# Kernel optimization log

Measured on AMD Instinct MI355X. Metric: run time of the kernel, lower is better.

The kernel has to match this reference:

```python
import jax, jax.numpy as jnp
from jax import lax
import numpy as np

N_E = 1024
E_DIM = 512
BETA = 0.25


def setup_inputs() -> dict:
    key = jax.random.key(0)
    k1, k2 = jax.random.split(key)
    z = jax.random.normal(k1, (16, 4096, E_DIM), dtype=jnp.float32)
    # torch init: uniform(-1/n_e, 1/n_e)
    codebook = jax.random.uniform(k2, (N_E, E_DIM), dtype=jnp.float32,
                                  minval=-1.0 / N_E, maxval=1.0 / N_E)
    return {"z": z, "codebook": codebook}


def reference(z, codebook):
    zf = z.reshape(-1, z.shape[-1])                      # (N, e_dim)
    # squared-distance matrix: ||z||^2 + ||e||^2 - 2 z e^T  -> (N, n_e)
    d = (jnp.sum(zf * zf, axis=1, keepdims=True)
         + jnp.sum(codebook * codebook, axis=1)
         - 2.0 * (zf @ codebook.T))
    idx = jnp.argmin(d, axis=1)                          # (N,)
    z_q = codebook[idx].reshape(z.shape)                 # (B, S, e_dim)
    loss = (jnp.mean((z_q - lax.stop_gradient(z)) ** 2)
            + BETA * jnp.mean((lax.stop_gradient(z_q) - z) ** 2))
    # straight-through estimator
    z_q_st = z + lax.stop_gradient(z_q - z)
    # perplexity of code usage (mean of one-hot == normalized counts)
    counts = jnp.zeros((codebook.shape[0],), dtype=z.dtype).at[idx].add(1.0)
    e_mean = counts / idx.shape[0]
    perplexity = jnp.exp(-jnp.sum(e_mean * jnp.log(e_mean + 1e-10)))
    return (loss, z_q_st, idx, perplexity)
```

## Files before the change

kernel.cpp:

```cpp
#include <hip/hip_runtime.h>
#include <hip/hip_bf16.h>

#define N_ROWS 65536
#define EDIM   512
#define NCODES 1024

#define WS_LOSS   0
#define WS_COUNTS 1
#define WS_ENORM  1025
#define WS_ZNORM  2049
#define WS_AMBCNT (2049 + 65536)
#define WS_WINNER (WS_AMBCNT + 1)
#define WS_AMBLST (WS_WINNER + 65536)
#define AMB_CAP   32768
#define WS_E2_OFF (1u << 20)
#define WS_FAST_BYTES (3u * 1024u * 1024u + 4096u)

#define AMB_EPS 1.6e-4f

typedef short short8 __attribute__((ext_vector_type(8)));
typedef float f32x4  __attribute__((ext_vector_type(4)));

#define AS1C(p) ((const __attribute__((address_space(1))) void*)(p))
#define AS3(p)  ((__attribute__((address_space(3))) void*)(p))

static __device__ __forceinline__ unsigned short f2bf(float f) {
    unsigned u = __float_as_uint(f);
    u += 0x7FFFu + ((u >> 16) & 1u);
    return (unsigned short)(u >> 16);
}
static __device__ __forceinline__ float bf2f(unsigned short h) {
    return __uint_as_float(((unsigned)h) << 16);
}

__global__ __launch_bounds__(256) void vq_prep(const float* __restrict__ cb,
                                               float* __restrict__ ws) {
    int j = blockIdx.x;
    int tid = threadIdx.x;
    float2 v = *(const float2*)&cb[(size_t)j * EDIM + tid * 2];
    float s = v.x * v.x + v.y * v.y;
    #pragma unroll
    for (int off = 32; off > 0; off >>= 1) s += __shfl_down(s, off);
    __shared__ float ls[4];
    int wave = tid >> 6, lane = tid & 63;
    if (lane == 0) ls[wave] = s;
    __syncthreads();
    if (tid == 0) {
        ws[WS_ENORM + j] = ls[0] + ls[1] + ls[2] + ls[3];
        ws[WS_COUNTS + j] = 0.0f;
        if (j == 0) {
            ws[WS_LOSS] = 0.0f;
            ((int*)ws)[WS_AMBCNT] = 0;
        }
    }
}

__global__ __launch_bounds__(256) void vq_znorm(const float* __restrict__ z,
                                                float* __restrict__ ws) {
    int tid  = threadIdx.x;
    int lrow = tid >> 5;
    int c    = tid & 31;
    long row = (long)blockIdx.x * 8 + lrow;
    const float* p = z + row * EDIM + (c >> 3) * 128 + (c & 7);
    float r = p[0] * p[0];
    #pragma unroll
    for (int i = 1; i < 16; ++i) {
        float v = p[i * 8];
        r += v * v;
    }
    r += __shfl_xor(r, 1);
    r += __shfl_xor(r, 2);
    r += __shfl_xor(r, 4);
    r += __shfl_xor(r, 8);
    r += __shfl_xor(r, 16);
    if (c == 0) ws[WS_ZNORM + row] = r;
}

__global__ __launch_bounds__(256) void vq_convz(const float* __restrict__ z,
                                                unsigned short* __restrict__ z2) {
    const int tid = threadIdx.x;
    const int p = blockIdx.x;
    const long row0 = (long)p * 128;
    const int row = tid >> 1, half = tid & 1;
    for (int kc = 0; kc < 16; ++kc) {
        const float* src = z + (row0 + row) * EDIM + kc * 32 + half * 16;
        float f[16];
        #pragma unroll
        for (int q = 0; q < 4; ++q) {
            float4 v = ((const float4*)src)[q];
            f[q*4+0] = v.x; f[q*4+1] = v.y; f[q*4+2] = v.z; f[q*4+3] = v.w;
        }
        unsigned hi[8], lo[8];
        #pragma unroll
        for (int q = 0; q < 8; ++q) {
            unsigned short h0 = f2bf(f[2*q]);
            unsigned short h1 = f2bf(f[2*q+1]);
            unsigned short l0 = f2bf(f[2*q]   - bf2f(h0));
            unsigned short l1 = f2bf(f[2*q+1] - bf2f(h1));
            hi[q] = (unsigned)h0 | ((unsigned)h1 << 16);
            lo[q] = (unsigned)l0 | ((unsigned)l1 << 16);
        }
        size_t base = ((size_t)(p * 16 + kc) * 2) * 4096;
        unsigned* dhi = (unsigned*)(z2 + base        + row * 32 + half * 16);
        unsigned* dlo = (unsigned*)(z2 + base + 4096 + row * 32 + half * 16);
        ((uint4*)dhi)[0] = make_uint4(hi[0], hi[1], hi[2], hi[3]);
        ((uint4*)dhi)[1] = make_uint4(hi[4], hi[5], hi[6], hi[7]);
        ((uint4*)dlo)[0] = make_uint4(lo[0], lo[1], lo[2], lo[3]);
        ((uint4*)dlo)[1] = make_uint4(lo[4], lo[5], lo[6], lo[7]);
    }
}

__global__ __launch_bounds__(256) void vq_convcb(const float* __restrict__ cb,
                                                 unsigned short* __restrict__ e2) {
    const int tid = threadIdx.x;
    const int cc = blockIdx.x;
    const int row = tid >> 1, half = tid & 1;
    for (int kc = 0; kc < 16; ++kc) {
        const float* src = cb + (size_t)(cc * 128 + row) * EDIM + kc * 32 + half * 16;
        float f[16];
        #pragma unroll
        for (int q = 0; q < 4; ++q) {
            float4 v = ((const float4*)src)[q];
            f[q*4+0] = v.x; f[q*4+1] = v.y; f[q*4+2] = v.z; f[q*4+3] = v.w;
        }
        unsigned hi[8], lo[8];
        #pragma unroll
        for (int q = 0; q < 8; ++q) {
            unsigned short h0 = f2bf(f[2*q]);
            unsigned short h1 = f2bf(f[2*q+1]);
            unsigned short l0 = f2bf(f[2*q]   - bf2f(h0));
            unsigned short l1 = f2bf(f[2*q+1] - bf2f(h1));
            hi[q] = (unsigned)h0 | ((unsigned)h1 << 16);
            lo[q] = (unsigned)l0 | ((unsigned)l1 << 16);
        }
        size_t base = ((size_t)(cc * 16 + kc) * 2) * 4096;
        unsigned* dhi = (unsigned*)(e2 + base        + row * 32 + half * 16);
        unsigned* dlo = (unsigned*)(e2 + base + 4096 + row * 32 + half * 16);
        ((uint4*)dhi)[0] = make_uint4(hi[0], hi[1], hi[2], hi[3]);
        ((uint4*)dhi)[1] = make_uint4(hi[4], hi[5], hi[6], hi[7]);
        ((uint4*)dlo)[0] = make_uint4(lo[0], lo[1], lo[2], lo[3]);
        ((uint4*)dlo)[1] = make_uint4(lo[4], lo[5], lo[6], lo[7]);
    }
}

__global__ __launch_bounds__(256, 2) void vq_mfma(const unsigned short* __restrict__ z2,
                                                  const unsigned short* __restrict__ e2,
                                                  const float* __restrict__ ws,
                                                  int* __restrict__ winner,
                                                  int* __restrict__ amb_count,
                                                  int* __restrict__ amb_list) {
    __shared__ unsigned short stage[16384];
    __shared__ float fv1[2][128];
    __shared__ float fv2[2][128];
    __shared__ int   fc1[2][128];

    const int tid = threadIdx.x;
    const int lane = tid & 63, w = tid >> 6;
    const int rw = (w & 1) * 64, cw = (w >> 1) * 64;
    const int ml = lane & 15, kg = lane >> 4;
    const long row0 = (long)blockIdx.x * 128;
    const float* __restrict__ enorm = ws + WS_ENORM;

    float v1[16], v2[16];
    int   c1[16];
    #pragma unroll
    for (int i = 0; i < 16; ++i) { v1[i] = INFINITY; v2[i] = INFINITY; c1[i] = 0; }

    const unsigned short* zt = stage;
    const unsigned short* et = stage + 8192;

    for (int cc = 0; cc < 8; ++cc) {
        f32x4 acc[4][4];
        #pragma unroll
        for (int rt = 0; rt < 4; ++rt)
            #pragma unroll
            for (int ct = 0; ct < 4; ++ct)
                acc[rt][ct] = (f32x4){0.f, 0.f, 0.f, 0.f};

        for (int kc = 0; kc < 16; ++kc) {
            __syncthreads();
            const uint4* zsrc = (const uint4*)(z2 + (size_t)(blockIdx.x * 16 + kc) * 8192);
            const uint4* esrc = (const uint4*)(e2 + (size_t)(cc * 16 + kc) * 8192);
            uint4* st = (uint4*)stage;
#if defined(__has_builtin) && __has_builtin(__builtin_amdgcn_global_load_lds)
            #pragma unroll
            for (int it = 0; it < 4; ++it) {
                int base = it * 256 + w * 64;
                __builtin_amdgcn_global_load_lds(AS1C(zsrc + base + lane), AS3(st + base), 16, 0, 0);
            }
            #pragma unroll
            for (int it = 0; it < 4; ++it) {
                int base = it * 256 + w * 64;
                __builtin_amdgcn_global_load_lds(AS1C(esrc + base + lane), AS3(st + 1024 + base), 16, 0, 0);
            }
#else
            #pragma unroll
            for (int it = 0; it < 4; ++it) {
                int i = it * 256 + tid;
                st[i] = zsrc[i];
            }
            #pragma unroll
            for (int it = 0; it < 4; ++it) {
                int i = it * 256 + tid;
                st[1024 + i] = esrc[i];
            }
#endif
            __syncthreads();

            short8 a[4][2], b[4][2];
            #pragma unroll
            for (int rt = 0; rt < 4; ++rt) {
                a[rt][0] = *(const short8*)&zt[        (rw + rt * 16 + ml) * 32 + kg * 8];
                a[rt][1] = *(const short8*)&zt[4096 + (rw + rt * 16 + ml) * 32 + kg * 8];
            }
            #pragma unroll
            for (int ct = 0; ct < 4; ++ct) {
                b[ct][0] = *(const short8*)&et[        (cw + ct * 16 + ml) * 32 + kg * 8];
                b[ct][1] = *(const short8*)&et[4096 + (cw + ct * 16 + ml) * 32 + kg * 8];
            }
            #pragma unroll
            for (int rt = 0; rt < 4; ++rt)
                #pragma unroll
                for (int ct = 0; ct < 4; ++ct) {
                    acc[rt][ct] = __builtin_amdgcn_mfma_f32_16x16x32_bf16(a[rt][0], b[ct][0], acc[rt][ct], 0, 0, 0);
                    acc[rt][ct] = __builtin_amdgcn_mfma_f32_16x16x32_bf16(a[rt][0], b[ct][1], acc[rt][ct], 0, 0, 0);
                    acc[rt][ct] = __builtin_amdgcn_mfma_f32_16x16x32_bf16(a[rt][1], b[ct][0], acc[rt][ct], 0, 0, 0);
                }
        }

        float en[4];
        #pragma unroll
        for (int ct = 0; ct < 4; ++ct) en[ct] = enorm[cc * 128 + cw + ct * 16 + ml];
        #pragma unroll
        for (int rt = 0; rt < 4; ++rt)
            #pragma unroll
            for (int ct = 0; ct < 4; ++ct) {
                int code = cc * 128 + cw + ct * 16 + ml;
                #pragma unroll
                for (int reg = 0; reg < 4; ++reg) {
                    float d = fmaf(-2.0f, acc[rt][ct][reg], en[ct]);
                    int i = rt * 4 + reg;
                    bool lt1 = d < v1[i];
                    bool lt2 = d < v2[i];
                    v2[i] = lt1 ? v1[i] : (lt2 ? d : v2[i]);
                    v1[i] = lt1 ? d : v1[i];
                    c1[i] = lt1 ? code : c1[i];
                }
            }
    }

    #pragma unroll
    for (int i = 0; i < 16; ++i) {
        #pragma unroll
        for (int off = 1; off < 16; off <<= 1) {
            float ov1 = __shfl_xor(v1[i], off);
            int   oc1 = __shfl_xor(c1[i], off);
            float ov2 = __shfl_xor(v2[i], off);
            bool take = (ov1 < v1[i]) || (ov1 == v1[i] && oc1 < c1[i]);
            float nv2 = take ? fminf(v1[i], ov2) : fminf(v2[i], ov1);
            v1[i] = take ? ov1 : v1[i];
            c1[i] = take ? oc1 : c1[i];
            v2[i] = nv2;
        }
    }
    __syncthreads();
    if (ml == 0) {
        #pragma unroll
        for (int i = 0; i < 16; ++i) {
            int row = rw + (i >> 2) * 16 + kg * 4 + (i & 3);
            fv1[w >> 1][row] = v1[i];
            fv2[w >> 1][row] = v2[i];
            fc1[w >> 1][row] = c1[i];
        }
    }
    __syncthreads();
    if (tid < 128) {
        float a1 = fv1[0][tid], a2 = fv2[0][tid];
        int   ac = fc1[0][tid];
        float b1 = fv1[1][tid], b2 = fv2[1][tid];
        int   bc = fc1[1][tid];
        bool take = (b1 < a1) || (b1 == a1 && bc < ac);
        float V1 = take ? b1 : a1;
        int   C1 = take ? bc : ac;
        float V2 = take ? fminf(a1, b2) : fminf(a2, b1);
        winner[row0 + tid] = C1;
        if (V2 - V1 < AMB_EPS) {
            int p = atomicAdd(amb_count, 1);
            if (p < AMB_CAP) amb_list[p] = (int)(row0 + tid);
        }
    }
}

#define RB 8
#define ZSR 9
__global__ __launch_bounds__(256) void vq_recheck(const float* __restrict__ z,
                                                  const float* __restrict__ cb,
                                                  const float* __restrict__ ws,
                                                  int* __restrict__ winner,
                                                  const int* __restrict__ amb_count,
                                                  const int* __restrict__ amb_list) {
    __shared__ float zs[EDIM * ZSR];
    __shared__ float wred_d[4];
    __shared__ int   wred_i[4];
    const int tid = threadIdx.x;
    const int lane = tid & 63, wv = tid >> 6;
    const float* __restrict__ enorm = ws + WS_ENORM;

    int n = *amb_count;
    bool overflow = (n > AMB_CAP);
    if (overflow) n = N_ROWS;
    int nIter = (n + RB - 1) / RB;

    const float* ec[4];
    float en4[4];
    #pragma unroll
    for (int c = 0; c < 4; ++c) {
        ec[c]  = cb + (size_t)(tid + 256 * c) * EDIM;
        en4[c] = enorm[tid + 256 * c];
    }

    for (int ii = blockIdx.x; ii < nIter; ii += gridDim.x) {
        int rows[RB];
        #pragma unroll
        for (int j = 0; j < RB; ++j) {
            int idx = ii * RB + j;
            if (idx >= n) idx = n - 1;
            rows[j] = overflow ? idx : amb_list[idx];
        }
        __syncthreads();
        #pragma unroll
        for (int j = 0; j < RB; ++j) {
            float2 v = *(const float2*)&z[(long)rows[j] * EDIM + tid * 2];
            zs[(tid * 2 + 0) * ZSR + j] = v.x;
            zs[(tid * 2 + 1) * ZSR + j] = v.y;
        }
        __syncthreads();

        float acc[RB][4];
        #pragma unroll
        for (int r = 0; r < RB; ++r)
            #pragma unroll
            for (int c = 0; c < 4; ++c) acc[r][c] = 0.0f;

        for (int k0 = 0; k0 < EDIM; k0 += 32) {
            float ain[RB][4];
            #pragma unroll
            for (int r = 0; r < RB; ++r)
                #pragma unroll
                for (int c = 0; c < 4; ++c) ain[r][c] = 0.0f;
            #pragma unroll
            for (int ks = 0; ks < 32; ks += 8) {
                float er[4][8];
                #pragma unroll
                for (int c = 0; c < 4; ++c) {
                    float4 a = *(const float4*)&ec[c][k0 + ks];
                    float4 b = *(const float4*)&ec[c][k0 + ks + 4];
                    er[c][0]=a.x; er[c][1]=a.y; er[c][2]=a.z; er[c][3]=a.w;
                    er[c][4]=b.x; er[c][5]=b.y; er[c][6]=b.z; er[c][7]=b.w;
                }
                #pragma unroll
                for (int kk = 0; kk < 8; ++kk) {
                    const float* zp = &zs[(k0 + ks + kk) * ZSR];
                    float4 z0 = *(const float4*)zp;
                    float4 z1 = *(const float4*)(zp + 4);
                    float zr[RB] = {z0.x, z0.y, z0.z, z0.w, z1.x, z1.y, z1.z, z1.w};
                    #pragma unroll
                    for (int r = 0; r < RB; ++r)
                        #pragma unroll
                        for (int c = 0; c < 4; ++c)
                            ain[r][c] = fmaf(zr[r], er[c][kk], ain[r][c]);
                }
            }
            #pragma unroll
            for (int r = 0; r < RB; ++r)
                #pragma unroll
                for (int c = 0; c < 4; ++c) acc[r][c] += ain[r][c];
        }

        #pragma unroll
        for (int r = 0; r < RB; ++r) {
            float zn = ws[WS_ZNORM + rows[r]];
            float bd = INFINITY;
            int   bc = 0;
            #pragma unroll
            for (int c = 0; c < 4; ++c) {
                float t = zn + en4[c];
                float d = t - 2.0f * acc[r][c];
                if (d < bd) { bd = d; bc = tid + 256 * c; }
            }
            #pragma unroll
            for (int off = 1; off < 64; off <<= 1) {
                float od = __shfl_xor(bd, off);
                int   oi = __shfl_xor(bc, off);
                if (od < bd || (od == bd && oi < bc)) { bd = od; bc = oi; }
            }
            if (lane == 0) { wred_d[wv] = bd; wred_i[wv] = bc; }
            __syncthreads();
            if (tid == 0) {
                float fd = wred_d[0]; int fi = wred_i[0];
                #pragma unroll
                for (int t2 = 1; t2 < 4; ++t2) {
                    if (wred_d[t2] < fd || (wred_d[t2] == fd && wred_i[t2] < fi)) {
                        fd = wred_d[t2]; fi = wred_i[t2];
                    }
                }
                winner[rows[r]] = fi;
            }
            __syncthreads();
        }
    }
}

__global__ __launch_bounds__(256) void vq_emit(const float* __restrict__ z,
                                               const float* __restrict__ cb,
                                               const int* __restrict__ winner,
                                               float* __restrict__ ws,
                                               float* __restrict__ out_zq,
                                               float* __restrict__ out_idx) {
    __shared__ float lred[4];
    const int tid = threadIdx.x;
    const long row0 = (long)blockIdx.x * 128;
    if (tid < 128) {
        int wi = winner[row0 + tid];
        out_idx[row0 + tid] = (float)wi;
        atomicAdd(&ws[WS_COUNTS + wi], 1.0f);
    }
    float lsum = 0.0f;
    for (int r = 0; r < 128; ++r) {
        int wv = winner[row0 + r];
        float2 e  = *(const float2*)&cb[(size_t)wv * EDIM + tid * 2];
        float2 zz = *(const float2*)&z[(row0 + r) * EDIM + tid * 2];
        float d0 = e.x - zz.x, d1 = e.y - zz.y;
        float2 o; o.x = zz.x + d0; o.y = zz.y + d1;
        *(float2*)&out_zq[(row0 + r) * EDIM + tid * 2] = o;
        lsum = fmaf(d0, d0, fmaf(d1, d1, lsum));
    }
    #pragma unroll
    for (int off = 32; off > 0; off >>= 1) lsum += __shfl_down(lsum, off);
    int wave = tid >> 6, lane = tid & 63;
    if (lane == 0) lred[wave] = lsum;
    __syncthreads();
    if (tid == 0) atomicAdd(&ws[WS_LOSS], lred[0] + lred[1] + lred[2] + lred[3]);
}

__global__ __launch_bounds__(1024) void vq_final(const float* __restrict__ ws,
                                                 float* __restrict__ out,
                                                 long off_perp) {
    int tid = threadIdx.x;
    float c = ws[WS_COUNTS + tid] * (1.0f / (float)N_ROWS);
    float t = c * logf(c + 1e-10f);
    #pragma unroll
    for (int off = 32; off > 0; off >>= 1) t += __shfl_down(t, off);
    __shared__ float ls[16];
    int wave = tid >> 6, lane = tid & 63;
    if (lane == 0) ls[wave] = t;
    __syncthreads();
    if (tid == 0) {
        float h = 0.0f;
        #pragma unroll
        for (int i = 0; i < 16; ++i) h += ls[i];
        out[off_perp] = expf(-h);
        out[0] = ws[WS_LOSS] * 1.25f / (float)((long)N_ROWS * EDIM);
    }
}

#define ROWS_PER_BLOCK 128
#define CODE_CHUNK     64
#define KCHUNK         32
#define ZSTRIDE        132
#define ESTRIDE        68

__global__ __launch_bounds__(256) void vq_main_fb(const float* __restrict__ z,
                                                  const float* __restrict__ cb,
                                                  float* __restrict__ ws,
                                                  float* __restrict__ out_zq,
                                                  float* __restrict__ out_idx) {
    __shared__ float zt[KCHUNK * ZSTRIDE];
    __shared__ float et[KCHUNK * ESTRIDE];
    __shared__ float red_d[ROWS_PER_BLOCK * 8];
    __shared__ int   red_i[ROWS_PER_BLOCK * 8];
    __shared__ int   winner[ROWS_PER_BLOCK];
    __shared__ float lred[4];

    const int tid = threadIdx.x;
    const int tx = tid & 7;
    const int ty = tid >> 3;
    const long row0 = (long)blockIdx.x * ROWS_PER_BLOCK;
    const float* __restrict__ enorm = ws + WS_ENORM;
    const float* __restrict__ znorm = ws + WS_ZNORM;

    float zn[4];
    #pragma unroll
    for (int i = 0; i < 4; ++i) zn[i] = znorm[row0 + ty * 4 + i];

    float best[4];
    int   bidx[4];
    #pragma unroll
    for (int i = 0; i < 4; ++i) { best[i] = INFINITY; bidx[i] = 0; }

    const int kq    = (tid & 7) * 4;
    const int rbase = tid >> 3;

    for (int c = 0; c < NCODES; c += CODE_CHUNK) {
        float acc[4][8];
        #pragma unroll
        for (int i = 0; i < 4; ++i)
            #pragma unroll
            for (int j = 0; j < 8; ++j) acc[i][j] = 0.0f;

        for (int k0 = 0; k0 < EDIM; k0 += KCHUNK) {
            __syncthreads();
            #pragma unroll
            for (int it = 0; it < 4; ++it) {
                int r = rbase + it * 32;
                float4 v = *(const float4*)&z[(row0 + r) * EDIM + k0 + kq];
                zt[(kq + 0) * ZSTRIDE + r] = v.x;
                zt[(kq + 1) * ZSTRIDE + r] = v.y;
                zt[(kq + 2) * ZSTRIDE + r] = v.z;
                zt[(kq + 3) * ZSTRIDE + r] = v.w;
            }
            #pragma unroll
            for (int it = 0; it < 2; ++it) {
                int e = rbase + it * 32;
                float4 v = *(const float4*)&cb[(size_t)(c + e) * EDIM + k0 + kq];
                et[(kq + 0) * ESTRIDE + e] = v.x;
                et[(kq + 1) * ESTRIDE + e] = v.y;
                et[(kq + 2) * ESTRIDE + e] = v.z;
                et[(kq + 3) * ESTRIDE + e] = v.w;
            }
            __syncthreads();
            float ain[4][8];
            #pragma unroll
            for (int i = 0; i < 4; ++i)
                #pragma unroll
                for (int j = 0; j < 8; ++j) ain[i][j] = 0.0f;
            #pragma unroll
            for (int kk = 0; kk < KCHUNK; ++kk) {
                float4 zv = *(const float4*)&zt[kk * ZSTRIDE + ty * 4];
                float4 e0 = *(const float4*)&et[kk * ESTRIDE + tx * 8];
                float4 e1 = *(const float4*)&et[kk * ESTRIDE + tx * 8 + 4];
                float za[4] = {zv.x, zv.y, zv.z, zv.w};
                float ea[8] = {e0.x, e0.y, e0.z, e0.w, e1.x, e1.y, e1.z, e1.w};
                #pragma unroll
                for (int i = 0; i < 4; ++i)
                    #pragma unroll
                    for (int j = 0; j < 8; ++j)
                        ain[i][j] = fmaf(za[i], ea[j], ain[i][j]);
            }
            #pragma unroll
            for (int i = 0; i < 4; ++i)
                #pragma unroll
                for (int j = 0; j < 8; ++j) acc[i][j] += ain[i][j];
        }
        #pragma unroll
        for (int j = 0; j < 8; ++j) {
            int code = c + tx * 8 + j;
            float en = enorm[code];
            #pragma unroll
            for (int i = 0; i < 4; ++i) {
                float t = zn[i] + en;
                float d = t - 2.0f * acc[i][j];
                if (d < best[i]) { best[i] = d; bidx[i] = code; }
            }
        }
    }

    __syncthreads();
    #pragma unroll
    for (int i = 0; i < 4; ++i) {
        red_d[(ty * 4 + i) * 8 + tx] = best[i];
        red_i[(ty * 4 + i) * 8 + tx] = bidx[i];
    }
    __syncthreads();
    if (tid < ROWS_PER_BLOCK) {
        float bd = red_d[tid * 8];
        int   bi = red_i[tid * 8];
        #pragma unroll
        for (int t = 1; t < 8; ++t) {
            float dv = red_d[tid * 8 + t];
            int   iv = red_i[tid * 8 + t];
            if (dv < bd || (dv == bd && iv < bi)) { bd = dv; bi = iv; }
        }
        winner[tid] = bi;
        out_idx[row0 + tid] = (float)bi;
        atomicAdd(&ws[WS_COUNTS + bi], 1.0f);
    }
    __syncthreads();

    float lsum = 0.0f;
    for (int r = 0; r < ROWS_PER_BLOCK; ++r) {
        int w = winner[r];
        float2 e  = *(const float2*)&cb[(size_t)w * EDIM + tid * 2];
        float2 zz = *(const float2*)&z[(row0 + r) * EDIM + tid * 2];
        float d0 = e.x - zz.x, d1 = e.y - zz.y;
        float2 o; o.x = zz.x + d0; o.y = zz.y + d1;
        *(float2*)&out_zq[(row0 + r) * EDIM + tid * 2] = o;
        lsum = fmaf(d0, d0, fmaf(d1, d1, lsum));
    }
    #pragma unroll
    for (int off = 32; off > 0; off >>= 1) lsum += __shfl_down(lsum, off);
    int wave = tid >> 6, lane = tid & 63;
    if (lane == 0) lred[wave] = lsum;
    __syncthreads();
    if (tid == 0) atomicAdd(&ws[WS_LOSS], lred[0] + lred[1] + lred[2] + lred[3]);
}

extern "C" void kernel_launch(void* const* d_in, const int* in_sizes, int n_in,
                              void* d_out, int out_size, void* d_ws, size_t ws_size,
                              hipStream_t stream) {
    const float* z  = (const float*)d_in[0];
    const float* cb = (const float*)d_in[1];
    float* out = (float*)d_out;
    float* ws  = (float*)d_ws;

    float* out_zq  = out + 1;
    float* out_idx = out + 1 + (long)N_ROWS * EDIM;
    long   off_perp = 1 + (long)N_ROWS * EDIM + N_ROWS;

    hipLaunchKernelGGL(vq_prep, dim3(NCODES), dim3(256), 0, stream, cb, ws);
    hipLaunchKernelGGL(vq_znorm, dim3(N_ROWS / 8), dim3(256), 0, stream, z, ws);

    if (ws_size >= (size_t)WS_FAST_BYTES) {
        unsigned short* z2 = (unsigned short*)(out + 4);
        unsigned short* e2 = (unsigned short*)((char*)d_ws + WS_E2_OFF);
        int* winner    = ((int*)ws) + WS_WINNER;
        int* amb_count = ((int*)ws) + WS_AMBCNT;
        int* amb_list  = ((int*)ws) + WS_AMBLST;

        hipLaunchKernelGGL(vq_convz, dim3(N_ROWS / 128), dim3(256), 0, stream, z, z2);
        hipLaunchKernelGGL(vq_convcb, dim3(8), dim3(256), 0, stream, cb, e2);
        hipLaunchKernelGGL(vq_mfma, dim3(N_ROWS / 128), dim3(256), 0, stream,
                           z2, e2, ws, winner, amb_count, amb_list);
        hipLaunchKernelGGL(vq_recheck, dim3(512), dim3(256), 0, stream,
                           z, cb, ws, winner, amb_count, amb_list);
        hipLaunchKernelGGL(vq_emit, dim3(N_ROWS / 128), dim3(256), 0, stream,
                           z, cb, winner, ws, out_zq, out_idx);
    } else {
        hipLaunchKernelGGL(vq_main_fb, dim3(N_ROWS / 128), dim3(256), 0, stream,
                           z, cb, ws, out_zq, out_idx);
    }
    hipLaunchKernelGGL(vq_final, dim3(1), dim3(1024), 0, stream, ws, out, off_perp);
}
```

Baseline: 698.9 us.

## Track top-3 distances to resolve two-way ties cheaply before full recheck

The MFMA pass now keeps the three smallest distances and two best codes per row. Rows whose runner-up is close but whose third candidate is not are sent to a new pairwise kernel that recomputes only those two fp32 dot products. Only rows with three or more near-ties go to the full-codebook recheck. The emit kernel also caches winners in LDS and uses float4 accesses. The extra top-3 bookkeeping adds register pressure and branching to the MFMA epilogue, and listA has no capacity guard.

```diff
diff --git a/kernel.cpp b/kernel.cpp
--- a/kernel.cpp
+++ b/kernel.cpp
@@ -9,10 +9,12 @@
 #define WS_COUNTS 1
 #define WS_ENORM  1025
 #define WS_ZNORM  2049
-#define WS_AMBCNT (2049 + 65536)
-#define WS_WINNER (WS_AMBCNT + 1)
-#define WS_AMBLST (WS_WINNER + 65536)
-#define AMB_CAP   32768
+#define WS_CNTA   67585
+#define WS_CNTB   67586
+#define WS_WINNER 67588
+#define WS_LISTA  133124
+#define WS_LISTB  198660
+#define CAPB      16384
 #define WS_E2_OFF (1u << 20)
 #define WS_FAST_BYTES (3u * 1024u * 1024u + 4096u)
 
@@ -31,6 +33,24 @@
 }
 static __device__ __forceinline__ float bf2f(unsigned short h) {
     return __uint_as_float(((unsigned)h) << 16);
+}
+
+static __device__ __forceinline__ bool lex_lt(float x, int cx, float y, int cy) {
+    return x < y || (x == y && cx < cy);
+}
+static __device__ __forceinline__ void merge3(float& a1, int& ac1, float& a2, int& ac2, float& a3,
+                                              float b1, int bc1, float b2, int bc2, float b3) {
+    float n1, n2, n3; int nc1, nc2;
+    if (lex_lt(b1, bc1, a1, ac1)) {
+        n1 = b1; nc1 = bc1;
+        if (lex_lt(a1, ac1, b2, bc2)) { n2 = a1; nc2 = ac1; n3 = fminf(a2, b2); }
+        else                          { n2 = b2; nc2 = bc2; n3 = fminf(a1, b3); }
+    } else {
+        n1 = a1; nc1 = ac1;
+        if (lex_lt(b1, bc1, a2, ac2)) { n2 = b1; nc2 = bc1; n3 = fminf(a2, b2); }
+        else                          { n2 = a2; nc2 = ac2; n3 = fminf(a3, b1); }
+    }
+    a1 = n1; ac1 = nc1; a2 = n2; ac2 = nc2; a3 = n3;
 }
 
 __global__ __launch_bounds__(256) void vq_prep(const float* __restrict__ cb,
@@ -50,7 +70,8 @@
         ws[WS_COUNTS + j] = 0.0f;
         if (j == 0) {
             ws[WS_LOSS] = 0.0f;
-            ((int*)ws)[WS_AMBCNT] = 0;
+            ((int*)ws)[WS_CNTA] = 0;
+            ((int*)ws)[WS_CNTB] = 0;
         }
     }
 }
@@ -147,12 +168,11 @@
                                                   const unsigned short* __restrict__ e2,
                                                   const float* __restrict__ ws,
                                                   int* __restrict__ winner,
-                                                  int* __restrict__ amb_count,
-                                                  int* __restrict__ amb_list) {
+                                                  int* __restrict__ cntA, int* __restrict__ listA,
+                                                  int* __restrict__ cntB, int* __restrict__ listB) {
     __shared__ unsigned short stage[16384];
-    __shared__ float fv1[2][128];
-    __shared__ float fv2[2][128];
-    __shared__ int   fc1[2][128];
+    __shared__ float fv1[2][128], fv2[2][128], fv3[2][128];
+    __shared__ int   fc1[2][128], fc2[2][128];
 
     const int tid = threadIdx.x;
     const int lane = tid & 63, w = tid >> 6;
@@ -161,10 +181,10 @@
     const long row0 = (long)blockIdx.x * 128;
     const float* __restrict__ enorm = ws + WS_ENORM;
 
-    float v1[16], v2[16];
-    int   c1[16];
-    #pragma unroll
-    for (int i = 0; i < 16; ++i) { v1[i] = INFINITY; v2[i] = INFINITY; c1[i] = 0; }
+    float v1[16], v2[16], v3[16];
+    int   c1[16], c2[16];
+    #pragma unroll
+    for (int i = 0; i < 16; ++i) { v1[i] = INFINITY; v2[i] = INFINITY; v3[i] = INFINITY; c1[i] = 0; c2[i] = 0; }
 
     const unsigned short* zt = stage;
     const unsigned short* et = stage + 8192;
@@ -195,15 +215,9 @@
             }
 #else
             #pragma unroll
-            for (int it = 0; it < 4; ++it) {
-                int i = it * 256 + tid;
-                st[i] = zsrc[i];
-            }
-            #pragma unroll
-            for (int it = 0; it < 4; ++it) {
-                int i = it * 256 + tid;
-                st[1024 + i] = esrc[i];
-            }
+            for (int it = 0; it < 4; ++it) { int i = it * 256 + tid; st[i] = zsrc[i]; }
+            #pragma unroll
+            for (int it = 0; it < 4; ++it) { int i = it * 256 + tid; st[1024 + i] = esrc[i]; }
 #endif
             __syncthreads();
 
@@ -240,11 +254,9 @@
                 for (int reg = 0; reg < 4; ++reg) {
                     float d = fmaf(-2.0f, acc[rt][ct][reg], en[ct]);
                     int i = rt * 4 + reg;
-                    bool lt1 = d < v1[i];
-                    bool lt2 = d < v2[i];
-                    v2[i] = lt1 ? v1[i] : (lt2 ? d : v2[i]);
-                    v1[i] = lt1 ? d : v1[i];
-                    c1[i] = lt1 ? code : c1[i];
+                    if (d < v1[i])      { v3[i] = v2[i]; v2[i] = v1[i]; c2[i] = c1[i]; v1[i] = d; c1[i] = code; }
+                    else if (d < v2[i]) { v3[i] = v2[i]; v2[i] = d; c2[i] = code; }
+                    else if (d < v3[i]) { v3[i] = d; }
                 }
             }
     }
@@ -253,14 +265,10 @@
     for (int i = 0; i < 16; ++i) {
         #pragma unroll
         for (int off = 1; off < 16; off <<= 1) {
-            float ov1 = __shfl_xor(v1[i], off);
-            int   oc1 = __shfl_xor(c1[i], off);
-            float ov2 = __shfl_xor(v2[i], off);
-            bool take = (ov1 < v1[i]) || (ov1 == v1[i] && oc1 < c1[i]);
-            float nv2 = take ? fminf(v1[i], ov2) : fminf(v2[i], ov1);
-            v1[i] = take ? ov1 : v1[i];
-            c1[i] = take ? oc1 : c1[i];
-            v2[i] = nv2;
+            float b1 = __shfl_xor(v1[i], off); int bc1 = __shfl_xor(c1[i], off);
+            float b2 = __shfl_xor(v2[i], off); int bc2 = __shfl_xor(c2[i], off);
+            float b3 = __shfl_xor(v3[i], off);
+            merge3(v1[i], c1[i], v2[i], c2[i], v3[i], b1, bc1, b2, bc2, b3);
         }
     }
     __syncthreads();
@@ -268,37 +276,80 @@
         #pragma unroll
         for (int i = 0; i < 16; ++i) {
             int row = rw + (i >> 2) * 16 + kg * 4 + (i & 3);
-            fv1[w >> 1][row] = v1[i];
-            fv2[w >> 1][row] = v2[i];
-            fc1[w >> 1][row] = c1[i];
+            int h = w >> 1;
+            fv1[h][row] = v1[i]; fv2[h][row] = v2[i]; fv3[h][row] = v3[i];
+            fc1[h][row] = c1[i]; fc2[h][row] = c2[i];
         }
     }
     __syncthreads();
     if (tid < 128) {
-        float a1 = fv1[0][tid], a2 = fv2[0][tid];
-        int   ac = fc1[0][tid];
-        float b1 = fv1[1][tid], b2 = fv2[1][tid];
-        int   bc = fc1[1][tid];
-        bool take = (b1 < a1) || (b1 == a1 && bc < ac);
-        float V1 = take ? b1 : a1;
-        int   C1 = take ? bc : ac;
-        float V2 = take ? fminf(a1, b2) : fminf(a2, b1);
-        winner[row0 + tid] = C1;
-        if (V2 - V1 < AMB_EPS) {
-            int p = atomicAdd(amb_count, 1);
-            if (p < AMB_CAP) amb_list[p] = (int)(row0 + tid);
+        float a1 = fv1[0][tid], a2 = fv2[0][tid], a3 = fv3[0][tid];
+        int   ac1 = fc1[0][tid], ac2 = fc2[0][tid];
+        merge3(a1, ac1, a2, ac2, a3,
+               fv1[1][tid], fc1[1][tid], fv2[1][tid], fc2[1][tid], fv3[1][tid]);
+        int row = (int)(row0 + tid);
+        winner[row] = ac1;
+        if (a2 - a1 < AMB_EPS) {
+            if (a3 - a1 >= AMB_EPS) {
+                int p = atomicAdd(cntA, 1);
+                listA[p] = (row << 10) | ac2;
+            } else {
+                int p = atomicAdd(cntB, 1);
+                if (p < CAPB) listB[p] = row;
+            }
+        }
+    }
+}
+
+__global__ __launch_bounds__(256) void vq_pair(const float* __restrict__ z,
+                                               const float* __restrict__ cb,
+                                               const float* __restrict__ ws,
+                                               int* __restrict__ winner,
+                                               const int* __restrict__ cntA,
+                                               const int* __restrict__ listA) {
+    int nA = *cntA;
+    int wid = blockIdx.x * 4 + (threadIdx.x >> 6);
+    int lane = threadIdx.x & 63;
+    int nw = gridDim.x * 4;
+    for (int i = wid; i < nA; i += nw) {
+        int e = listA[i];
+        int row = e >> 10, cB = e & 1023;
+        int cA = winner[row];
+        int j = (lane >> 4) & 1;
+        int ck = lane & 15;
+        int code = j ? cB : cA;
+        const float* zp = z + (long)row * EDIM + ck * 32;
+        const float* ep = cb + (size_t)code * EDIM + ck * 32;
+        float ain = 0.0f;
+        #pragma unroll
+        for (int q = 0; q < 8; ++q) {
+            float4 zv = *(const float4*)&zp[q * 4];
+            float4 ev = *(const float4*)&ep[q * 4];
+            ain = fmaf(zv.x, ev.x, ain);
+            ain = fmaf(zv.y, ev.y, ain);
+            ain = fmaf(zv.z, ev.z, ain);
+            ain = fmaf(zv.w, ev.w, ain);
+        }
+        float s0 = __shfl(ain, 0), s1 = __shfl(ain, 16);
+        #pragma unroll
+        for (int c = 1; c < 16; ++c) { s0 += __shfl(ain, c); s1 += __shfl(ain, 16 + c); }
+        if (lane == 0) {
+            float zn = ws[WS_ZNORM + row];
+            float d1 = (zn + ws[WS_ENORM + cA]) - 2.0f * s0;
+            float d2 = (zn + ws[WS_ENORM + cB]) - 2.0f * s1;
+            winner[row] = lex_lt(d2, cB, d1, cA) ? cB : cA;
         }
     }
 }
 
 #define RB 8
 #define ZSR 9
-__global__ __launch_bounds__(256) void vq_recheck(const float* __restrict__ z,
-                                                  const float* __restrict__ cb,
-                                                  const float* __restrict__ ws,
-                                                  int* __restrict__ winner,
-                                                  const int* __restrict__ amb_count,
-                                                  const int* __restrict__ amb_list) {
+__global__ __launch_bounds__(256) void vq_full(const float* __restrict__ z,
+                                               const float* __restrict__ cb,
+                                               const float* __restrict__ ws,
+                                               int* __restrict__ winner,
+                                               const int* __restrict__ cntB,
+                                               const int* __restrict__ listB) {
     __shared__ float zs[EDIM * ZSR];
     __shared__ float wred_d[4];
     __shared__ int   wred_i[4];
@@ -306,8 +357,8 @@
     const int lane = tid & 63, wv = tid >> 6;
     const float* __restrict__ enorm = ws + WS_ENORM;
 
-    int n = *amb_count;
-    bool overflow = (n > AMB_CAP);
+    int n = *cntB;
+    bool overflow = (n > CAPB);
     if (overflow) n = N_ROWS;
     int nIter = (n + RB - 1) / RB;
 
@@ -325,7 +376,7 @@
         for (int j = 0; j < RB; ++j) {
             int idx = ii * RB + j;
             if (idx >= n) idx = n - 1;
-            rows[j] = overflow ? idx : amb_list[idx];
+            rows[j] = overflow ? idx : listB[idx];
         }
         __syncthreads();
         #pragma unroll
@@ -418,22 +469,29 @@
                                                float* __restrict__ out_zq,
                                                float* __restrict__ out_idx) {
     __shared__ float lred[4];
+    __shared__ int wlds[128];
     const int tid = threadIdx.x;
     const long row0 = (long)blockIdx.x * 128;
     if (tid < 128) {
         int wi = winner[row0 + tid];
+        wlds[tid] = wi;
         out_idx[row0 + tid] = (float)wi;
         atomicAdd(&ws[WS_COUNTS + wi], 1.0f);
     }
+    __syncthreads();
     float lsum = 0.0f;
-    for (int r = 0; r < 128; ++r) {
-        int wv = winner[row0 + r];
-        float2 e  = *(const float2*)&cb[(size_t)wv * EDIM + tid * 2];
-        float2 zz = *(const float2*)&z[(row0 + r) * EDIM + tid * 2];
-        float d0 = e.x - zz.x, d1 = e.y - zz.y;
-        float2 o; o.x = zz.x + d0; o.y = zz.y + d1;
-        *(float2*)&out_zq[(row0 + r) * EDIM + tid * 2] = o;
-        lsum = fmaf(d0, d0, fmaf(d1, d1, lsum));
+    const int sub = tid >> 7;
+    const int col = (tid & 127) * 4;
+    for (int it = 0; it < 64; ++it) {
+        int r = it * 2 + sub;
+        int wv = wlds[r];
+        float4 e  = *(const float4*)&cb[(size_t)wv * EDIM + col];
+        float4 zz = *(const float4*)&z[(row0 + r) * EDIM + col];
+        float d0 = e.x - zz.x, d1 = e.y - zz.y, d2 = e.z - zz.z, d3 = e.w - zz.w;
+        float4 o;
+        o.x = zz.x + d0; o.y = zz.y + d1; o.z = zz.z + d2; o.w = zz.w + d3;
+        *(float4*)&out_zq[(row0 + r) * EDIM + col] = o;
+        lsum = fmaf(d0, d0, fmaf(d1, d1, fmaf(d2, d2, fmaf(d3, d3, lsum))));
     }
     #pragma unroll
     for (int off = 32; off > 0; off >>= 1) lsum += __shfl_down(lsum, off);
@@ -623,16 +681,20 @@
     if (ws_size >= (size_t)WS_FAST_BYTES) {
         unsigned short* z2 = (unsigned short*)(out + 4);
         unsigned short* e2 = (unsigned short*)((char*)d_ws + WS_E2_OFF);
-        int* winner    = ((int*)ws) + WS_WINNER;
-        int* amb_count = ((int*)ws) + WS_AMBCNT;
-        int* amb_list  = ((int*)ws) + WS_AMBLST;
+        int* winner = ((int*)ws) + WS_WINNER;
+        int* cntA   = ((int*)ws) + WS_CNTA;
+        int* cntB   = ((int*)ws) + WS_CNTB;
+        int* listA  = ((int*)ws) + WS_LISTA;
+        int* listB  = ((int*)ws) + WS_LISTB;
 
         hipLaunchKernelGGL(vq_convz, dim3(N_ROWS / 128), dim3(256), 0, stream, z, z2);
         hipLaunchKernelGGL(vq_convcb, dim3(8), dim3(256), 0, stream, cb, e2);
         hipLaunchKernelGGL(vq_mfma, dim3(N_ROWS / 128), dim3(256), 0, stream,
-                           z2, e2, ws, winner, amb_count, amb_list);
-        hipLaunchKernelGGL(vq_recheck, dim3(512), dim3(256), 0, stream,
-                           z, cb, ws, winner, amb_count, amb_list);
+                           z2, e2, ws, winner, cntA, listA, cntB, listB);
+        hipLaunchKernelGGL(vq_pair, dim3(256), dim3(256), 0, stream,
+                           z, cb, ws, winner, cntA, listA);
+        hipLaunchKernelGGL(vq_full, dim3(512), dim3(256), 0, stream,
+                           z, cb, ws, winner, cntB, listB);
         hipLaunchKernelGGL(vq_emit, dim3(N_ROWS / 128), dim3(256), 0, stream,
                            z, cb, winner, ws, out_zq, out_idx);
     } else {
```

New measurement: 749.9 us. +7.3%, slower.
